# Performance work log

Measured on AMD Instinct MI355X. Metric: run time of the kernel, lower is better.

Reference implementation:

```python
import jax, jax.numpy as jnp
import numpy as np

BLANK = 1   # Offsets.GO
NEG = -1e30  # effective -inf that stays finite under logaddexp


def setup_inputs() -> dict:
    key = jax.random.key(0)
    k1, k2, k3, k4 = jax.random.split(key, 4)
    T, B, V, S = 1000, 64, 512, 100
    logits = jax.random.normal(k1, (T, B, V), dtype=jnp.float32)
    log_prob = jax.nn.log_softmax(logits, axis=-1)  # ctc_loss expects log-probs
    input_lengths = jax.random.randint(k2, (B,), T // 2, T + 1, dtype=jnp.int32)
    # target tokens avoid PAD(0)/GO(1,blank)/EOS(2), matching the masked_select semantics
    targets = jax.random.randint(k3, (B, S), 3, V, dtype=jnp.int32)
    target_lengths = jax.random.randint(k4, (B,), S // 2, S + 1, dtype=jnp.int32)
    return {"log_prob": log_prob, "input_lengths": input_lengths,
            "targets": targets, "target_lengths": target_lengths}


def _ctc_loss_sum(log_prob, input_lengths, targets, target_lengths):
    # log_prob: (T, B, V) log-softmax outputs; targets: (B, S) padded labels
    T, B, V = log_prob.shape
    S = targets.shape[1]
    Se = 2 * S + 1  # extended label sequence: blank-interleaved

    ext = jnp.full((B, Se), BLANK, dtype=targets.dtype).at[:, 1::2].set(targets)
    pos = jnp.arange(Se)
    ext_len = 2 * target_lengths + 1                      # (B,)
    valid = pos[None, :] < ext_len[:, None]               # (B, Se)
    ext_m2 = jnp.pad(ext[:, :-2], ((0, 0), (2, 0)), constant_values=BLANK)
    allow_skip = (ext != BLANK) & (ext != ext_m2) & (pos[None, :] >= 2)

    # emit[t, b, s] = log_prob[t, b, ext[b, s]]  -> (T, B, Se)
    emit = jnp.take_along_axis(log_prob, jnp.broadcast_to(ext[None], (T, B, Se)), axis=2)

    # alpha init at t=0
    alpha = jnp.full((B, Se), NEG, dtype=log_prob.dtype)
    alpha = alpha.at[:, 0].set(emit[0, :, 0])
    alpha = alpha.at[:, 1].set(jnp.where(target_lengths > 0, emit[0, :, 1], NEG))
    alpha = jnp.where(valid, alpha, NEG)

    def step(alpha, xt):
        emit_t, t = xt
        a1 = alpha
        a2 = jnp.pad(alpha[:, :-1], ((0, 0), (1, 0)), constant_values=NEG)
        a3 = jnp.where(allow_skip,
                       jnp.pad(alpha[:, :-2], ((0, 0), (2, 0)), constant_values=NEG),
                       NEG)
        new = jnp.logaddexp(jnp.logaddexp(a1, a2), a3) + emit_t
        new = jnp.where(valid, new, NEG)
        # freeze alpha once past each sample's input length
        alpha = jnp.where((t < input_lengths)[:, None], new, alpha)
        return alpha, None

    alpha, _ = jax.lax.scan(step, alpha, (emit[1:], jnp.arange(1, T)))

    last = 2 * target_lengths  # index of trailing blank in extended sequence
    a_last = jnp.take_along_axis(alpha, last[:, None], axis=1)[:, 0]
    a_prev = jnp.take_along_axis(alpha, jnp.maximum(last - 1, 0)[:, None], axis=1)[:, 0]
    loglik = jnp.logaddexp(a_last, a_prev)
    loss = -loglik
    # zero_infinity=True: infeasible alignments contribute 0
    loss = jnp.where(loglik < 0.5 * NEG, 0.0, loss)
    return jnp.sum(loss)  # reduction='sum'


def reference(log_prob, input_lengths, targets, target_lengths):
    return _ctc_loss_sum(log_prob, input_lengths, targets, target_lengths)
```

## Files before the change

kernel.cpp:

```cpp
#include <hip/hip_runtime.h>


#define NEGF (-1e30f)

constexpr int CT_T  = 1000;
constexpr int CT_B  = 64;
constexpr int CT_V  = 512;
constexpr int CT_S  = 100;
constexpr int CT_Se = 201;
constexpr float LOG2E = 1.4426950408889634f;
constexpr float LN2   = 0.6931471805599453f;
constexpr float SHIFT = 5.0f;

typedef float f4 __attribute__((ext_vector_type(4)));

#if __has_builtin(__builtin_amdgcn_exp2f) && __has_builtin(__builtin_amdgcn_logf)
__device__ __forceinline__ float fexp2(float x) { return __builtin_amdgcn_exp2f(x); }
__device__ __forceinline__ float flog2(float x) { return __builtin_amdgcn_logf(x); }
__device__ __forceinline__ float frcp(float x)  { return __builtin_amdgcn_rcpf(x); }
#else
__device__ __forceinline__ float fexp2(float x) { return exp2f(x); }
__device__ __forceinline__ float flog2(float x) { return log2f(x); }
__device__ __forceinline__ float frcp(float x)  { return 1.0f / x; }
#endif

__device__ __forceinline__ float lae2_b2(float x, float y) {
    float m = fmaxf(x, y);
    float d = fminf(x, y) - m;
    return m + flog2(1.0f + fexp2(d));
}
__device__ __forceinline__ float lae3_b2(float x, float y, float z) {
    float m = fmaxf(fmaxf(x, y), z);
    float s = fexp2(x - m) + fexp2(y - m) + fexp2(z - m);
    return m + flog2(s);
}

__device__ __forceinline__ float wave_shr1(float x) {
    return __int_as_float(__builtin_amdgcn_update_dpp(
        0, __float_as_int(x), 0x138, 0xf, 0xf, true));
}
__device__ __forceinline__ float wave_max_nonneg(float x) {
#define DPPMAX(ctrl) x = fmaxf(x, __int_as_float(__builtin_amdgcn_update_dpp( \
        0, __float_as_int(x), ctrl, 0xf, 0xf, true)))
    DPPMAX(0x111); DPPMAX(0x112); DPPMAX(0x114); DPPMAX(0x118);
    DPPMAX(0x142); DPPMAX(0x143);
#undef DPPMAX
    return __int_as_float(__builtin_amdgcn_readlane(__float_as_int(x), 63));
}

typedef const __attribute__((address_space(1))) unsigned int* as1_uint_ptr;
typedef __attribute__((address_space(3))) unsigned int* as3_uint_ptr;
__device__ __forceinline__ void gld16(const void* g, void* l) {
    __builtin_amdgcn_global_load_lds((as1_uint_ptr)g, (as3_uint_ptr)l, 16, 0, 0);
}
__device__ __forceinline__ void gld4(const void* g, void* l) {
    __builtin_amdgcn_global_load_lds((as1_uint_ptr)g, (as3_uint_ptr)l, 4, 0, 0);
}

#define WAIT_VM0() do { \
    asm volatile("s_waitcnt vmcnt(0)" ::: "memory"); \
    __builtin_amdgcn_sched_barrier(0); } while (0)
#define DRAIN_LGKM() asm volatile("s_waitcnt lgkmcnt(0)" ::: "memory")

__global__ __launch_bounds__(256, 1) void ctc_alpha_pp(
    const float* __restrict__ logp,
    const int*   __restrict__ in_len,
    const int*   __restrict__ tgt,
    const int*   __restrict__ tgt_len,
    float*       __restrict__ loss_ws)
{
    __shared__ __align__(16) float stage[8][8][192];
    __shared__ __align__(16) float hand[272];

    const int b    = blockIdx.x;
    const int tid  = threadIdx.x;
    const int wv   = tid >> 6;
    const int lane = tid & 63;
    const int Tin  = in_len[b];
    const int Lt   = tgt_len[b];
    const int lim  = 2 * Lt + 1;
    const int* tg  = tgt + b * CT_S;

    const int K  = (Tin - 1 + 7) / 8;
    const int NT = (Tin - 1 + 15) / 16;

    const int s0 = 4 * lane, s1 = s0 + 1, s3 = s0 + 3;
    const int i1 = min((s1 - 1) >> 1, CT_S - 1);
    const int i3 = min((s3 - 1) >> 1, CT_S - 1);
    const int c1 = tg[i1];
    const int c3 = tg[i3];
    const float sk1 = ((s1 >= 3) && (s1 < CT_Se) && (c1 != tg[max(i1 - 1, 0)])) ? 1.f : 0.f;
    const float sk3 = ((s3 >= 3) && (s3 < CT_Se) && (c3 != tg[max(i3 - 1, 0)])) ? 1.f : 0.f;
    const float m0 = (s0     < lim) ? 1.f : 0.f;
    const float m2 = (s0 + 2 < lim) ? 1.f : 0.f;
    const float Sy = (s0 + 1 < lim) ? SHIFT : -1000.f;
    const float Sw = (s0 + 3 < lim) ? SHIFT : -1000.f;

    float a0 = 0.f, a1 = 0.f, a2 = 0.f, a3 = 0.f, pa3 = 0.f;
    if (tid == 0) {
        const float* r0 = logp + (size_t)b * CT_V;
        a0 = fexp2(fmaf(r0[1], LOG2E, SHIFT));
        if (Lt > 0) a1 = fexp2(fmaf(r0[c1], LOG2E, SHIFT));
    }
    float rs = 0.f;

    float ex[16], ey[16], ez[16], ew[16];

    auto issue = [&](int c) {
        if (c >= K) return;
        const int buf = c & 7, tb = 1 + 8 * c;
        #pragma unroll
        for (int i = 0; i < 8; ++i) {
            const int t = min(tb + i, CT_T - 1);
            const float* r = logp + ((size_t)t * CT_B + b) * CT_V;
            gld4(r + c1, &stage[buf][i][0]);
            gld4(r + c3, &stage[buf][i][64]);
            gld4(r + 1,  &stage[buf][i][128]);
        }
    };

    auto read24 = [&](int c, float (&g)[24]) {
        unsigned base = (unsigned)(size_t)(&stage[c & 7][0][0]) + 4u * (unsigned)lane;
        asm volatile(
            "ds_read_b32 %0,  %24 offset:0\n\t"
            "ds_read_b32 %1,  %24 offset:256\n\t"
            "ds_read_b32 %2,  %24 offset:512\n\t"
            "ds_read_b32 %3,  %24 offset:768\n\t"
            "ds_read_b32 %4,  %24 offset:1024\n\t"
            "ds_read_b32 %5,  %24 offset:1280\n\t"
            "ds_read_b32 %6,  %24 offset:1536\n\t"
            "ds_read_b32 %7,  %24 offset:1792\n\t"
            "ds_read_b32 %8,  %24 offset:2048\n\t"
            "ds_read_b32 %9,  %24 offset:2304\n\t"
            "ds_read_b32 %10, %24 offset:2560\n\t"
            "ds_read_b32 %11, %24 offset:2816\n\t"
            "ds_read_b32 %12, %24 offset:3072\n\t"
            "ds_read_b32 %13, %24 offset:3328\n\t"
            "ds_read_b32 %14, %24 offset:3584\n\t"
            "ds_read_b32 %15, %24 offset:3840\n\t"
            "ds_read_b32 %16, %24 offset:4096\n\t"
            "ds_read_b32 %17, %24 offset:4352\n\t"
            "ds_read_b32 %18, %24 offset:4608\n\t"
            "ds_read_b32 %19, %24 offset:4864\n\t"
            "ds_read_b32 %20, %24 offset:5120\n\t"
            "ds_read_b32 %21, %24 offset:5376\n\t"
            "ds_read_b32 %22, %24 offset:5632\n\t"
            "ds_read_b32 %23, %24 offset:5888\n\t"
            "s_waitcnt lgkmcnt(0)"
            : "=&v"(g[0]), "=&v"(g[1]), "=&v"(g[2]), "=&v"(g[3]), "=&v"(g[4]),
              "=&v"(g[5]), "=&v"(g[6]), "=&v"(g[7]), "=&v"(g[8]), "=&v"(g[9]),
              "=&v"(g[10]), "=&v"(g[11]), "=&v"(g[12]), "=&v"(g[13]),
              "=&v"(g[14]), "=&v"(g[15]), "=&v"(g[16]), "=&v"(g[17]),
              "=&v"(g[18]), "=&v"(g[19]), "=&v"(g[20]), "=&v"(g[21]),
              "=&v"(g[22]), "=&v"(g[23])
            : "v"(base));
        __builtin_amdgcn_sched_barrier(0);
    };

    auto prep2 = [&](int c0) {
        float gA[24], gB[24];
        read24(c0, gA);
        read24(c0 + 1, gB);
        #pragma unroll
        for (int s = 0; s < 16; ++s) {
            const float* g = (s < 8) ? &gA[3 * s] : &gB[3 * (s - 8)];
            float e1 = fexp2(fmaf(g[0], LOG2E, Sy));
            float e3 = fexp2(fmaf(g[1], LOG2E, Sw));
            float eb = fexp2(fmaf(g[2], LOG2E, SHIFT));
            ex[s] = eb * m0; ey[s] = e1; ez[s] = eb * m2; ew[s] = e3;
        }
    };

    auto renorm = [&]() {
        float lm = wave_max_nonneg(fmaxf(fmaxf(a0, a1), fmaxf(a2, a3)));
        if (lm > 0.f) {
            float sc = frcp(lm);
            rs += flog2(lm);
            a0 *= sc; a1 *= sc; a2 *= sc; a3 *= sc;
            pa3 = wave_shr1(a3);
        }
    };

    auto recurse = [&](int i) {
        if (i > 0) {
            f4 h = *reinterpret_cast<f4*>(&hand[4 * lane]);
            a0 = h.x; a1 = h.y; a2 = h.z; a3 = h.w;
            rs = hand[256];
            pa3 = wave_shr1(a3);
        }
        const int tb = 1 + 16 * i;
        const bool guard = (16 * i + 16 > Tin - 1);
        #pragma unroll
        for (int s = 0; s < 16; ++s) {
            float n0 = (a0 + pa3) * ex[s];
            float n1 = fmaf(sk1, pa3, a1 + a0) * ey[s];
            float n2 = (a2 + a1) * ez[s];
            float n3 = fmaf(sk3, a1, a3 + a2) * ew[s];
            if (!guard || (tb + s < Tin)) { a0 = n0; a1 = n1; a2 = n2; a3 = n3; }
            pa3 = wave_shr1(a3);
        }
        renorm();
        f4 h; h.x = a0; h.y = a1; h.z = a2; h.w = a3;
        *reinterpret_cast<f4*>(&hand[4 * lane]) = h;
        if (lane == 0) hand[256] = rs;
        DRAIN_LGKM();
    };

    if (wv == 2) { WAIT_VM0(); issue(0); issue(1); issue(2); issue(3); WAIT_VM0(); }
    else if (wv == 3) { WAIT_VM0(); issue(4); issue(5); }
    __builtin_amdgcn_s_barrier();
    if (wv == 0) prep2(0);
    __builtin_amdgcn_s_barrier();

    for (int i = 0; i < NT; ++i) {
        if (wv < 2) {
            if ((i & 1) == wv)      recurse(i);
            else if (i + 1 < NT)    prep2(2 * i + 2);
        } else {
            const int p = wv - 2;
            if ((i & 1) == p) { issue(2 * i + 6); issue(2 * i + 7); }
            else              { WAIT_VM0(); }
        }
        __builtin_amdgcn_s_barrier();
    }

    if (wv >= 2) {
        asm volatile("s_waitcnt vmcnt(0)" ::: "memory");
        return;
    }
    if (wv != ((NT - 1) & 1)) return;

    const int last = 2 * Lt;
    const int prev = max(last - 1, 0);
    const int lr = last & 3, lidx = last >> 2;
    float av = (lr == 0) ? a0 : (lr == 1) ? a1 : (lr == 2) ? a2 : a3;
    float a_last = __shfl(av, lidx);
    const int pr = prev & 3, pidx = prev >> 2;
    float pv = (pr == 0) ? a0 : (pr == 1) ? a1 : (pr == 2) ? a2 : a3;
    float a_prev = __shfl(pv, pidx);

    float sum = a_last + a_prev;
    float loss = 0.f;
    if (sum > 0.f)
        loss = -(flog2(sum) + rs - SHIFT * (float)Tin) * LN2;
    if (lane == 0) loss_ws[b] = loss;
}

__global__ __launch_bounds__(64) void ctc_alpha_fb(
    const float* __restrict__ logp, const int* __restrict__ in_len,
    const int* __restrict__ tgt, const int* __restrict__ tgt_len,
    float* __restrict__ loss_ws)
{
    const int b = blockIdx.x, lane = threadIdx.x;
    const int Tin = in_len[b], Lt = tgt_len[b];
    const int ext_len = 2 * Lt + 1;
    const int* tg = tgt + b * CT_S;
    const int s0 = 4 * lane, s1 = s0 + 1, s3 = s0 + 3;
    const int i1 = min((s1 - 1) >> 1, CT_S - 1);
    const int i3 = min((s3 - 1) >> 1, CT_S - 1);
    const int c1 = tg[i1], c3 = tg[i3];
    const bool skip1 = (s1 >= 3) && (s1 < CT_Se) && (c1 != tg[max(i1 - 1, 0)]);
    const bool skip3 = (s3 >= 3) && (s3 < CT_Se) && (c3 != tg[max(i3 - 1, 0)]);
    const bool v0 = s0 < ext_len, v1 = s1 < ext_len;
    const bool v2 = (s0 + 2) < ext_len, v3 = s3 < ext_len;
    const float* row0 = logp + (long long)b * CT_V;
    const long long stride = (long long)CT_B * CT_V;
    float a0 = NEGF, a1 = NEGF, a2 = NEGF, a3 = NEGF;
    if (lane == 0) {
        a0 = row0[1] * LOG2E;
        if (ext_len > 1) a1 = row0[c1] * LOG2E;
    }
    float3 E0, E1, E2, E3;
    auto ld = [&](float3& e, int t) {
        int tt = min(t, CT_T - 1);
        const float* r = row0 + (long long)tt * stride;
        e.x = r[1] * LOG2E; e.y = r[c1] * LOG2E; e.z = r[c3] * LOG2E;
    };
    auto step = [&](const float3& e) {
        float pa3 = __shfl_up(a3, 1);
        if (lane == 0) pa3 = NEGF;
        float z1 = skip1 ? pa3 : NEGF;
        float z3 = skip3 ? a1 : NEGF;
        float n0 = v0 ? lae2_b2(a0, pa3)    + e.x : NEGF;
        float n1 = v1 ? lae3_b2(a1, a0, z1) + e.y : NEGF;
        float n2 = v2 ? lae2_b2(a2, a1)     + e.x : NEGF;
        float n3 = v3 ? lae3_b2(a3, a2, z3) + e.z : NEGF;
        a0 = n0; a1 = n1; a2 = n2; a3 = n3;
    };
    ld(E0, 1); ld(E1, 2); ld(E2, 3); ld(E3, 4);
    for (int t = 1; t < Tin; t += 4) {
        step(E0); ld(E0, t + 4);
        if (t + 1 < Tin) { step(E1); ld(E1, t + 5); }
        if (t + 2 < Tin) { step(E2); ld(E2, t + 6); }
        if (t + 3 < Tin) { step(E3); ld(E3, t + 7); }
    }
    const int last = 2 * Lt, prev = max(last - 1, 0);
    const int lr = last & 3, lidx = last >> 2;
    float av = (lr == 0) ? a0 : (lr == 1) ? a1 : (lr == 2) ? a2 : a3;
    float a_last = __shfl(av, lidx);
    const int pr = prev & 3, pidx = prev >> 2;
    float pv = (pr == 0) ? a0 : (pr == 1) ? a1 : (pr == 2) ? a2 : a3;
    float a_prev = __shfl(pv, pidx);
    float loglik = lae2_b2(a_last, a_prev) * LN2;
    float loss = (loglik < 0.5f * NEGF) ? 0.0f : -loglik;
    if (lane == 0) loss_ws[b] = loss;
}

__global__ __launch_bounds__(64) void ctc_sum(const float* __restrict__ loss_ws,
                                              float* __restrict__ out)
{
    float v = loss_ws[threadIdx.x];
    #pragma unroll
    for (int o = 32; o > 0; o >>= 1) v += __shfl_down(v, o);
    if (threadIdx.x == 0) out[0] = v;
}

extern "C" void kernel_launch(void* const* d_in, const int* in_sizes, int n_in,
                              void* d_out, int out_size, void* d_ws, size_t ws_size,
                              hipStream_t stream) {
    const float* logp    = (const float*)d_in[0];
    const int*   in_len  = (const int*)d_in[1];
    const int*   tgt     = (const int*)d_in[2];
    const int*   tgt_len = (const int*)d_in[3];
    float* out = (float*)d_out;
    float* loss_ws = (float*)d_ws;

    if (ws_size >= 256 * sizeof(float)) {
        hipLaunchKernelGGL(ctc_alpha_pp, dim3(CT_B), dim3(256), 0, stream,
                           logp, in_len, tgt, tgt_len, loss_ws);
    } else {
        hipLaunchKernelGGL(ctc_alpha_fb, dim3(CT_B), dim3(64), 0, stream,
                           logp, in_len, tgt, tgt_len, loss_ws);
    }
    hipLaunchKernelGGL(ctc_sum, dim3(1), dim3(64), 0, stream, loss_ws, out);
}
```

Baseline: 203.1 us.

## Stage full vocab rows via 16-byte LDS loads with double-buffered 15-step tiles

Replaces the per-lane 4-byte gathers of three emission values per timestep with coalesced 16-byte global-to-LDS copies of whole 512-float vocabulary rows. Tile size drops from 16 to 15 steps with a two-deep buffer instead of an eight-deep one, and both loader waves now split each tile's rows and wait every iteration. The gather then happens from LDS in prep. This trades many small scattered loads for roughly 2.7x more bytes moved per step and a shallower prefetch queue.

```diff
diff --git a/kernel.cpp b/kernel.cpp
--- a/kernel.cpp
+++ b/kernel.cpp
@@ -8,6 +8,7 @@
 constexpr int CT_V  = 512;
 constexpr int CT_S  = 100;
 constexpr int CT_Se = 201;
+constexpr int RT    = 15;
 constexpr float LOG2E = 1.4426950408889634f;
 constexpr float LN2   = 0.6931471805599453f;
 constexpr float SHIFT = 5.0f;
@@ -53,9 +54,6 @@
 __device__ __forceinline__ void gld16(const void* g, void* l) {
     __builtin_amdgcn_global_load_lds((as1_uint_ptr)g, (as3_uint_ptr)l, 16, 0, 0);
 }
-__device__ __forceinline__ void gld4(const void* g, void* l) {
-    __builtin_amdgcn_global_load_lds((as1_uint_ptr)g, (as3_uint_ptr)l, 4, 0, 0);
-}
 
 #define WAIT_VM0() do { \
     asm volatile("s_waitcnt vmcnt(0)" ::: "memory"); \
@@ -69,8 +67,8 @@
     const int*   __restrict__ tgt_len,
     float*       __restrict__ loss_ws)
 {
-    __shared__ __align__(16) float stage[8][8][192];
-    __shared__ __align__(16) float hand[272];
+    __shared__ __align__(16) float stage[2][RT][CT_V];
+    __shared__ __align__(16) float hand[260];
 
     const int b    = blockIdx.x;
     const int tid  = threadIdx.x;
@@ -81,8 +79,7 @@
     const int lim  = 2 * Lt + 1;
     const int* tg  = tgt + b * CT_S;
 
-    const int K  = (Tin - 1 + 7) / 8;
-    const int NT = (Tin - 1 + 15) / 16;
+    const int NT = (Tin - 1 + RT - 1) / RT;
 
     const int s0 = 4 * lane, s1 = s0 + 1, s3 = s0 + 3;
     const int i1 = min((s1 - 1) >> 1, CT_S - 1);
@@ -104,70 +101,35 @@
     }
     float rs = 0.f;
 
-    float ex[16], ey[16], ez[16], ew[16];
+    float ex[RT], ey[RT], ez[RT], ew[RT];
+
+    const int rb = (wv == 3) ? 8 : 0;
+    const int re = (wv == 3) ? RT : 8;
 
     auto issue = [&](int c) {
-        if (c >= K) return;
-        const int buf = c & 7, tb = 1 + 8 * c;
+        const int tb = 1 + RT * c;
+        const int buf = c & 1;
+        for (int r = rb; r < re; ++r) {
+            const int t = min(tb + r, CT_T - 1);
+            const char* g = (const char*)(logp + ((size_t)t * CT_B + b) * CT_V)
+                          + (size_t)lane * 16;
+            gld16(g,        &stage[buf][r][0]);
+            gld16(g + 1024, &stage[buf][r][256]);
+        }
+    };
+
+    auto prep = [&](int tn) {
+        const int buf = tn & 1;
         #pragma unroll
-        for (int i = 0; i < 8; ++i) {
-            const int t = min(tb + i, CT_T - 1);
-            const float* r = logp + ((size_t)t * CT_B + b) * CT_V;
-            gld4(r + c1, &stage[buf][i][0]);
-            gld4(r + c3, &stage[buf][i][64]);
-            gld4(r + 1,  &stage[buf][i][128]);
-        }
-    };
-
-    auto read24 = [&](int c, float (&g)[24]) {
-        unsigned base = (unsigned)(size_t)(&stage[c & 7][0][0]) + 4u * (unsigned)lane;
-        asm volatile(
-            "ds_read_b32 %0,  %24 offset:0\n\t"
-            "ds_read_b32 %1,  %24 offset:256\n\t"
-            "ds_read_b32 %2,  %24 offset:512\n\t"
-            "ds_read_b32 %3,  %24 offset:768\n\t"
-            "ds_read_b32 %4,  %24 offset:1024\n\t"
-            "ds_read_b32 %5,  %24 offset:1280\n\t"
-            "ds_read_b32 %6,  %24 offset:1536\n\t"
-            "ds_read_b32 %7,  %24 offset:1792\n\t"
-            "ds_read_b32 %8,  %24 offset:2048\n\t"
-            "ds_read_b32 %9,  %24 offset:2304\n\t"
-            "ds_read_b32 %10, %24 offset:2560\n\t"
-            "ds_read_b32 %11, %24 offset:2816\n\t"
-            "ds_read_b32 %12, %24 offset:3072\n\t"
-            "ds_read_b32 %13, %24 offset:3328\n\t"
-            "ds_read_b32 %14, %24 offset:3584\n\t"
-            "ds_read_b32 %15, %24 offset:3840\n\t"
-            "ds_read_b32 %16, %24 offset:4096\n\t"
-            "ds_read_b32 %17, %24 offset:4352\n\t"
-            "ds_read_b32 %18, %24 offset:4608\n\t"
-            "ds_read_b32 %19, %24 offset:4864\n\t"
-            "ds_read_b32 %20, %24 offset:5120\n\t"
-            "ds_read_b32 %21, %24 offset:5376\n\t"
-            "ds_read_b32 %22, %24 offset:5632\n\t"
-            "ds_read_b32 %23, %24 offset:5888\n\t"
-            "s_waitcnt lgkmcnt(0)"
-            : "=&v"(g[0]), "=&v"(g[1]), "=&v"(g[2]), "=&v"(g[3]), "=&v"(g[4]),
-              "=&v"(g[5]), "=&v"(g[6]), "=&v"(g[7]), "=&v"(g[8]), "=&v"(g[9]),
-              "=&v"(g[10]), "=&v"(g[11]), "=&v"(g[12]), "=&v"(g[13]),
-              "=&v"(g[14]), "=&v"(g[15]), "=&v"(g[16]), "=&v"(g[17]),
-              "=&v"(g[18]), "=&v"(g[19]), "=&v"(g[20]), "=&v"(g[21]),
-              "=&v"(g[22]), "=&v"(g[23])
-            : "v"(base));
-        __builtin_amdgcn_sched_barrier(0);
-    };
-
-    auto prep2 = [&](int c0) {
-        float gA[24], gB[24];
-        read24(c0, gA);
-        read24(c0 + 1, gB);
-        #pragma unroll
-        for (int s = 0; s < 16; ++s) {
-            const float* g = (s < 8) ? &gA[3 * s] : &gB[3 * (s - 8)];
-            float e1 = fexp2(fmaf(g[0], LOG2E, Sy));
-            float e3 = fexp2(fmaf(g[1], LOG2E, Sw));
-            float eb = fexp2(fmaf(g[2], LOG2E, SHIFT));
-            ex[s] = eb * m0; ey[s] = e1; ez[s] = eb * m2; ew[s] = e3;
+        for (int s = 0; s < RT; ++s) {
+            float gb = stage[buf][s][1];
+            float g1 = stage[buf][s][c1];
+            float g3 = stage[buf][s][c3];
+            float eb = fexp2(fmaf(gb, LOG2E, SHIFT));
+            ey[s] = fexp2(fmaf(g1, LOG2E, Sy));
+            ew[s] = fexp2(fmaf(g3, LOG2E, Sw));
+            ex[s] = eb * m0;
+            ez[s] = eb * m2;
         }
     };
 
@@ -188,10 +150,10 @@
             rs = hand[256];
             pa3 = wave_shr1(a3);
         }
-        const int tb = 1 + 16 * i;
-        const bool guard = (16 * i + 16 > Tin - 1);
+        const int tb = 1 + RT * i;
+        const bool guard = (tb + RT > Tin);
         #pragma unroll
-        for (int s = 0; s < 16; ++s) {
+        for (int s = 0; s < RT; ++s) {
             float n0 = (a0 + pa3) * ex[s];
             float n1 = fmaf(sk1, pa3, a1 + a0) * ey[s];
             float n2 = (a2 + a1) * ez[s];
@@ -206,28 +168,27 @@
         DRAIN_LGKM();
     };
 
-    if (wv == 2) { WAIT_VM0(); issue(0); issue(1); issue(2); issue(3); WAIT_VM0(); }
-    else if (wv == 3) { WAIT_VM0(); issue(4); issue(5); }
+    if (wv >= 2) {
+        WAIT_VM0();
+        issue(0); issue(1);
+        WAIT_VM0();
+    }
     __builtin_amdgcn_s_barrier();
-    if (wv == 0) prep2(0);
+    if (wv == 0) prep(0);
     __builtin_amdgcn_s_barrier();
 
     for (int i = 0; i < NT; ++i) {
         if (wv < 2) {
-            if ((i & 1) == wv)      recurse(i);
-            else if (i + 1 < NT)    prep2(2 * i + 2);
+            if ((i & 1) == wv)   recurse(i);
+            else if (i + 1 < NT) prep(i + 1);
         } else {
-            const int p = wv - 2;
-            if ((i & 1) == p) { issue(2 * i + 6); issue(2 * i + 7); }
-            else              { WAIT_VM0(); }
+            if (i + 2 < NT) issue(i + 2);
+            WAIT_VM0();
         }
         __builtin_amdgcn_s_barrier();
     }
 
-    if (wv >= 2) {
-        asm volatile("s_waitcnt vmcnt(0)" ::: "memory");
-        return;
-    }
+    if (wv >= 2) return;
     if (wv != ((NT - 1) & 1)) return;
 
     const int last = 2 * Lt;
```

Measured after the change: 225.1 us. 1.11x slower.
